# Optimization experiments

Hardware: AMD Instinct MI355X
Metric: run time of the kernel (lower is better)

## Reference

```python
import jax, jax.numpy as jnp
import numpy as np

E, T, H, I = 16, 4, 512, 1024  # expert_num, task_num, hidden_size, input_size
B = 8192


def setup_inputs() -> dict:
    key = jax.random.key(0)
    ks = jax.random.split(key, 8)
    s_i = 1.0 / np.sqrt(I)
    s_h = 1.0 / np.sqrt(H)
    return {
        "x": jax.random.normal(ks[0], (B, I), dtype=jnp.float32),
        "We": jax.random.uniform(ks[1], (E, H, I), jnp.float32, -s_i, s_i),
        "be": jax.random.uniform(ks[2], (E, H), jnp.float32, -s_i, s_i),
        "Wg": jax.random.uniform(ks[3], (T, E, I), jnp.float32, -s_i, s_i),
        "bg": jax.random.uniform(ks[4], (T, E), jnp.float32, -s_i, s_i),
        "Wf": jax.random.uniform(ks[5], (T, H), jnp.float32, -s_h, s_h),
        "bf": jax.random.uniform(ks[6], (T,), jnp.float32, -s_h, s_h),
    }


def reference(x, We, be, Wg, bg, Wf, bf):
    # expert outputs: relu(x @ We_e^T + be_e)  -> [B, E, H]
    eo = jax.nn.relu(jnp.einsum("bi,ehi->beh", x, We) + be[None])
    # gate outputs: softmax over experts        -> [B, T, E]
    g = jax.nn.softmax(jnp.einsum("bi,tei->bte", x, Wg) + bg[None], axis=-1)
    # gated combine                             -> [T, B, H]
    res = jnp.einsum("bte,beh->tbh", g, eo)
    # per-task scalar heads                     -> [T, B, 1]
    out = jnp.einsum("tbh,th->tb", res, Wf) + bf[:, None]
    return out[:, :, None]
```

## Files before the change

kernel.cpp:

```cpp
#include <hip/hip_runtime.h>
#include <hip/hip_bf16.h>
#include <stdint.h>


#define E_ 16
#define T_ 4
#define H_ 512
#define I_ 1024
#define B_ 8192
#define N_ (E_ * H_)
#define K_ I_

typedef __bf16 bf16x8 __attribute__((ext_vector_type(8)));
typedef float f32x4 __attribute__((ext_vector_type(4)));

__device__ __forceinline__ unsigned short f2bf_rne(float f) {
  unsigned int b = __float_as_uint(f);
  b += 0x7fffu + ((b >> 16) & 1u);
  return (unsigned short)(b >> 16);
}

#define N4X (B_ * K_ / 4)
#define N4W (N_ * K_ / 4)
#define N4G (64 * K_ / 4)

__global__ __launch_bounds__(256) void cvt3_kernel(const float* __restrict__ x,
                                                   const float* __restrict__ We,
                                                   const float* __restrict__ Wg,
                                                   unsigned short* __restrict__ xb,
                                                   unsigned short* __restrict__ wb,
                                                   unsigned short* __restrict__ wgb) {
  int i = blockIdx.x * 256 + threadIdx.x;
  const float* src;
  unsigned short* dst;
  int j;
  if (i < N4X) {
    src = x; dst = xb; j = i;
  } else if (i < N4X + N4W) {
    src = We; dst = wb; j = i - N4X;
  } else if (i < N4X + N4W + N4G) {
    src = Wg; dst = wgb; j = i - (N4X + N4W);
  } else {
    return;
  }
  float4 v = reinterpret_cast<const float4*>(src)[j];
  ushort4 o;
  o.x = f2bf_rne(v.x);
  o.y = f2bf_rne(v.y);
  o.z = f2bf_rne(v.z);
  o.w = f2bf_rne(v.w);
  reinterpret_cast<ushort4*>(dst)[j] = o;
}

__device__ __forceinline__ void gld_lds16(const void* gp, void* lp) {
  __builtin_amdgcn_global_load_lds((const __attribute__((address_space(1))) void*)gp,
                                   (__attribute__((address_space(3))) void*)lp, 16, 0, 0);
}

__global__ __launch_bounds__(256) void logits_softmax_kernel(
    const unsigned short* __restrict__ A,
    const unsigned short* __restrict__ Bm,
    const float* __restrict__ bg,
    float* __restrict__ g)
{
  __shared__ struct {
    unsigned short A[128 * 32];
    unsigned short B[64 * 32];
  } st;

  const int tid = threadIdx.x;
  const int w = tid >> 6, l = tid & 63;
  const int m16 = l & 15, q = l >> 4;
  const size_t m0 = (size_t)blockIdx.x * 128;

  const int r0s = (w * 2 + 0) * 16 + (l >> 2);
  const int r1s = (w * 2 + 1) * 16 + (l >> 2);
  const int slot = l & 3;
  const int c0 = slot ^ ((r0s >> 1) & 3);
  const int c1 = slot ^ ((r1s >> 1) & 3);
  const size_t offA0 = (m0 + r0s) * K_ + c0 * 8;
  const size_t offA1 = (m0 + r1s) * K_ + c1 * 8;
  const int l0 = (w * 2 + 0) * 512;
  const int l1 = (w * 2 + 1) * 512;
  const int rBs = w * 16 + (l >> 2);
  const int cB = slot ^ ((rBs >> 1) & 3);
  const size_t offB = (size_t)rBs * K_ + cB * 8;
  const int lB = w * 512;

  const int arow = w * 32 + m16;
  const int sA = q ^ ((arow >> 1) & 3);
  const int sB = q ^ ((m16 >> 1) & 3);

  f32x4 acc[2][4] = {};

  for (int k0 = 0; k0 < K_; k0 += 32) {
    __syncthreads();
    gld_lds16(A + offA0 + k0, st.A + l0);
    gld_lds16(A + offA1 + k0, st.A + l1);
    gld_lds16(Bm + offB + k0, st.B + lB);
    __syncthreads();
    bf16x8 af[2], bfr[4];
#pragma unroll
    for (int i = 0; i < 2; ++i)
      af[i] = *reinterpret_cast<const bf16x8*>(st.A + (arow + i * 16) * 32 + sA * 8);
#pragma unroll
    for (int j = 0; j < 4; ++j)
      bfr[j] = *reinterpret_cast<const bf16x8*>(st.B + (j * 16 + m16) * 32 + sB * 8);
#pragma unroll
    for (int i = 0; i < 2; ++i)
#pragma unroll
      for (int j = 0; j < 4; ++j)
        acc[i][j] = __builtin_amdgcn_mfma_f32_16x16x32_bf16(af[i], bfr[j], acc[i][j], 0, 0, 0);
  }

  float bgv[4];
#pragma unroll
  for (int j = 0; j < 4; ++j) bgv[j] = bg[j * 16 + m16];

#pragma unroll
  for (int i = 0; i < 2; ++i) {
    float lg[4][4];
#pragma unroll
    for (int j = 0; j < 4; ++j)
#pragma unroll
      for (int r = 0; r < 4; ++r) lg[r][j] = acc[i][j][r] + bgv[j];
#pragma unroll
    for (int r = 0; r < 4; ++r) {
#pragma unroll
      for (int j = 0; j < 4; ++j) {
        float m = lg[r][j];
#pragma unroll
        for (int mask = 1; mask < 16; mask <<= 1) m = fmaxf(m, __shfl_xor(m, mask, 64));
        float ex = __expf(lg[r][j] - m);
        float s = ex;
#pragma unroll
        for (int mask = 1; mask < 16; mask <<= 1) s += __shfl_xor(s, mask, 64);
        size_t b = m0 + w * 32 + i * 16 + q * 4 + r;
        g[b * 64 + j * 16 + m16] = ex / s;
      }
    }
  }
}

__global__ __launch_bounds__(256, 2) void moe_main_kernel(
    const unsigned short* __restrict__ A,
    const unsigned short* __restrict__ Bm,
    const float* __restrict__ be,
    const float* __restrict__ Wf,
    const float* __restrict__ g,
    float* __restrict__ partials)
{
  __shared__ union {
    struct {
      unsigned short A0[128 * 32];
      unsigned short A1[128 * 32];
      unsigned short B0[128 * 32];
      unsigned short B1[128 * 32];
    } st;
    float allsums[2 * 512];
  } sm;

  const int tid = threadIdx.x;
  const int w = tid >> 6, l = tid & 63;
  const int wm = w >> 1, wn = w & 1;
  const int m16 = l & 15, q = l >> 4;
  const int nb = blockIdx.x, mb = blockIdx.y;
  const size_t m0 = (size_t)mb * 128, n0 = (size_t)nb * 128;

  const int r0s = (w * 2 + 0) * 16 + (l >> 2);
  const int r1s = (w * 2 + 1) * 16 + (l >> 2);
  const int slot = l & 3;
  const int c0 = slot ^ ((r0s >> 1) & 3);
  const int c1 = slot ^ ((r1s >> 1) & 3);
  const size_t offA0 = (m0 + r0s) * K_ + c0 * 8;
  const size_t offA1 = (m0 + r1s) * K_ + c1 * 8;
  const size_t offB0 = (n0 + r0s) * K_ + c0 * 8;
  const size_t offB1 = (n0 + r1s) * K_ + c1 * 8;
  const int l0 = (w * 2 + 0) * 512;
  const int l1 = (w * 2 + 1) * 512;

  const int arow = wm * 64 + m16;
  const int brow = wn * 64 + m16;
  const int sA = q ^ ((arow >> 1) & 3);
  const int sB = q ^ ((brow >> 1) & 3);

  f32x4 acc[4][4] = {};

  for (int k0 = 0; k0 < K_; k0 += 64) {
    __syncthreads();
    gld_lds16(A + offA0 + k0, sm.st.A0 + l0);
    gld_lds16(A + offA1 + k0, sm.st.A0 + l1);
    gld_lds16(A + offA0 + k0 + 32, sm.st.A1 + l0);
    gld_lds16(A + offA1 + k0 + 32, sm.st.A1 + l1);
    gld_lds16(Bm + offB0 + k0, sm.st.B0 + l0);
    gld_lds16(Bm + offB1 + k0, sm.st.B0 + l1);
    gld_lds16(Bm + offB0 + k0 + 32, sm.st.B1 + l0);
    gld_lds16(Bm + offB1 + k0 + 32, sm.st.B1 + l1);
    __syncthreads();
#pragma unroll
    for (int h = 0; h < 2; ++h) {
      const unsigned short* bufA = h ? sm.st.A1 : sm.st.A0;
      const unsigned short* bufB = h ? sm.st.B1 : sm.st.B0;
      bf16x8 af[4], bfr[4];
#pragma unroll
      for (int i = 0; i < 4; ++i)
        af[i] = *reinterpret_cast<const bf16x8*>(bufA + (arow + i * 16) * 32 + sA * 8);
#pragma unroll
      for (int j = 0; j < 4; ++j)
        bfr[j] = *reinterpret_cast<const bf16x8*>(bufB + (brow + j * 16) * 32 + sB * 8);
#pragma unroll
      for (int i = 0; i < 4; ++i)
#pragma unroll
        for (int j = 0; j < 4; ++j)
          acc[i][j] = __builtin_amdgcn_mfma_f32_16x16x32_bf16(af[i], bfr[j], acc[i][j], 0, 0, 0);
    }
  }

  __syncthreads();

  const int hbase = (int)(n0 & 511);

  float wfv[4][4];
#pragma unroll
  for (int t = 0; t < 4; ++t)
#pragma unroll
    for (int j = 0; j < 4; ++j)
      wfv[t][j] = Wf[t * H_ + hbase + wn * 64 + j * 16 + m16];
  float bias[4];
#pragma unroll
  for (int j = 0; j < 4; ++j) bias[j] = be[n0 + wn * 64 + j * 16 + m16];

  const int reg_sel = m16 >> 2, t_sel = m16 & 3;
#pragma unroll
  for (int i = 0; i < 4; ++i) {
    float eo[4][4];
#pragma unroll
    for (int j = 0; j < 4; ++j)
#pragma unroll
      for (int r = 0; r < 4; ++r) eo[j][r] = fmaxf(acc[i][j][r] + bias[j], 0.f);
    float p[16];
#pragma unroll
    for (int r = 0; r < 4; ++r)
#pragma unroll
      for (int t = 0; t < 4; ++t) {
        float v = 0.f;
#pragma unroll
        for (int j = 0; j < 4; ++j) v += eo[j][r] * wfv[t][j];
        p[r * 4 + t] = v;
      }
#pragma unroll
    for (int mask = 1; mask < 16; mask <<= 1)
#pragma unroll
      for (int s = 0; s < 16; ++s) p[s] += __shfl_xor(p[s], mask, 64);
    float v = p[0];
#pragma unroll
    for (int s = 1; s < 16; ++s) v = (m16 == s) ? p[s] : v;
    int row = wm * 64 + i * 16 + q * 4 + reg_sel;
    sm.allsums[wn * 512 + row * 4 + t_sel] = v;
  }
  __syncthreads();

  const int e_idx = (int)(n0 >> 9);
#pragma unroll
  for (int oi = 0; oi < 2; ++oi) {
    int o = tid * 2 + oi;
    int row = o >> 2, t = o & 3;
    float s = sm.allsums[row * 4 + t] + sm.allsums[512 + row * 4 + t];
    size_t b = m0 + row;
    float gv = g[b * 64 + t * 16 + e_idx];
    partials[(size_t)nb * (T_ * B_) + (size_t)t * B_ + b] = gv * s;
  }
}

__global__ __launch_bounds__(128) void reduce_kernel(const float* __restrict__ partials,
                                                     const float* __restrict__ bfv,
                                                     float* __restrict__ out) {
  int i = blockIdx.x * 128 + threadIdx.x;
  float s = bfv[i >> 13];
#pragma unroll 4
  for (int nb = 0; nb < 64; ++nb) s += partials[(size_t)nb * (T_ * B_) + i];
  out[i] = s;
}

extern "C" void kernel_launch(void* const* d_in, const int* in_sizes, int n_in,
                              void* d_out, int out_size, void* d_ws, size_t ws_size,
                              hipStream_t stream) {
  const float* x = (const float*)d_in[0];
  const float* We = (const float*)d_in[1];
  const float* be = (const float*)d_in[2];
  const float* Wg = (const float*)d_in[3];
  const float* bg = (const float*)d_in[4];
  const float* Wf = (const float*)d_in[5];
  const float* bf = (const float*)d_in[6];
  float* out = (float*)d_out;

  unsigned short* xb = (unsigned short*)d_ws;
  unsigned short* wb = xb + (size_t)B_ * K_;
  unsigned short* wgb = wb + (size_t)N_ * K_;
  float* g = (float*)(wgb + (size_t)64 * K_);
  float* partials = g + (size_t)B_ * 64;

  cvt3_kernel<<<(N4X + N4W + N4G + 255) / 256, 256, 0, stream>>>(x, We, Wg, xb, wb, wgb);
  logits_softmax_kernel<<<B_ / 128, 256, 0, stream>>>(xb, wgb, bg, g);
  dim3 grid(N_ / 128, B_ / 128);
  moe_main_kernel<<<grid, 256, 0, stream>>>(xb, wb, be, Wf, g, partials);
  reduce_kernel<<<(T_ * B_) / 128, 128, 0, stream>>>(partials, bf, out);
}
```

Baseline: 291.3 us.

## Double-buffer LDS tiles to overlap global loads with MFMA compute

Stages the A and B k-tiles through two LDS buffers: the first tile is loaded before the main loop, and each iteration issues the async global-to-LDS loads for the next k-tile before running MFMAs on the current one. This cuts the barriers per k-step from two to one and aims to hide global load latency behind compute. In exchange, shared memory for the staging area doubles to 64KB per block, which with two blocks per CU puts more pressure on LDS capacity.

New measurement: 303.6 us. 1.04x slower.

```diff
diff --git a/kernel.cpp b/kernel.cpp
--- a/kernel.cpp
+++ b/kernel.cpp
@@ -152,10 +152,8 @@
 {
   __shared__ union {
     struct {
-      unsigned short A0[128 * 32];
-      unsigned short A1[128 * 32];
-      unsigned short B0[128 * 32];
-      unsigned short B1[128 * 32];
+      unsigned short A[2][2][128 * 32];
+      unsigned short B[2][2][128 * 32];
     } st;
     float allsums[2 * 512];
   } sm;
@@ -186,21 +184,33 @@
 
   f32x4 acc[4][4] = {};
 
-  for (int k0 = 0; k0 < K_; k0 += 64) {
-    __syncthreads();
-    gld_lds16(A + offA0 + k0, sm.st.A0 + l0);
-    gld_lds16(A + offA1 + k0, sm.st.A0 + l1);
-    gld_lds16(A + offA0 + k0 + 32, sm.st.A1 + l0);
-    gld_lds16(A + offA1 + k0 + 32, sm.st.A1 + l1);
-    gld_lds16(Bm + offB0 + k0, sm.st.B0 + l0);
-    gld_lds16(Bm + offB1 + k0, sm.st.B0 + l1);
-    gld_lds16(Bm + offB0 + k0 + 32, sm.st.B1 + l0);
-    gld_lds16(Bm + offB1 + k0 + 32, sm.st.B1 + l1);
-    __syncthreads();
+#pragma unroll
+  for (int h = 0; h < 2; ++h) {
+    gld_lds16(A + offA0 + h * 32, sm.st.A[0][h] + l0);
+    gld_lds16(A + offA1 + h * 32, sm.st.A[0][h] + l1);
+    gld_lds16(Bm + offB0 + h * 32, sm.st.B[0][h] + l0);
+    gld_lds16(Bm + offB1 + h * 32, sm.st.B[0][h] + l1);
+  }
+  __syncthreads();
+
+  for (int it = 0; it < K_ / 64; ++it) {
+    const int p = it & 1;
+    const int k0 = it * 64;
+    if (k0 + 64 < K_) {
+      const int np = 1 - p;
+      const int kn = k0 + 64;
+#pragma unroll
+      for (int h = 0; h < 2; ++h) {
+        gld_lds16(A + offA0 + kn + h * 32, sm.st.A[np][h] + l0);
+        gld_lds16(A + offA1 + kn + h * 32, sm.st.A[np][h] + l1);
+        gld_lds16(Bm + offB0 + kn + h * 32, sm.st.B[np][h] + l0);
+        gld_lds16(Bm + offB1 + kn + h * 32, sm.st.B[np][h] + l1);
+      }
+    }
 #pragma unroll
     for (int h = 0; h < 2; ++h) {
-      const unsigned short* bufA = h ? sm.st.A1 : sm.st.A0;
-      const unsigned short* bufB = h ? sm.st.B1 : sm.st.B0;
+      const unsigned short* bufA = sm.st.A[p][h];
+      const unsigned short* bufB = sm.st.B[p][h];
       bf16x8 af[4], bfr[4];
 #pragma unroll
       for (int i = 0; i < 4; ++i)
@@ -214,9 +224,8 @@
         for (int j = 0; j < 4; ++j)
           acc[i][j] = __builtin_amdgcn_mfma_f32_16x16x32_bf16(af[i], bfr[j], acc[i][j], 0, 0, 0);
     }
-  }
-
-  __syncthreads();
+    __syncthreads();
+  }
 
   const int hbase = (int)(n0 & 511);
 
```
